# Performance work log

Hardware: AMD Instinct MI355X
Metric: run time of the kernel (lower is better)

## Reference

```python
import jax, jax.numpy as jnp
import numpy as np


def setup_inputs() -> dict:
    key = jax.random.key(0)
    ks = jax.random.split(key, 7)
    T, K, D_x, D_y = 8192, 64, 128, 64
    X = jax.random.normal(ks[0], (T, D_x), dtype=jnp.float32)
    Y = jax.random.normal(ks[1], (T, D_y), dtype=jnp.float32)
    # learned parameters (small random values for non-degenerate math)
    init_logits = jax.random.normal(ks[2], (K,), dtype=jnp.float32) * 0.1
    W = jax.random.normal(ks[3], (K, K, D_x), dtype=jnp.float32) * 0.05
    b = jax.random.normal(ks[4], (K, K), dtype=jnp.float32) * 0.1
    mu = jax.random.normal(ks[5], (K, D_y), dtype=jnp.float32) * 0.1
    log_var_unconstrained = jax.random.normal(ks[6], (K, D_y), dtype=jnp.float32) * 0.1
    return {"X": X, "Y": Y, "init_logits": init_logits, "W": W, "b": b,
            "mu": mu, "log_var_unconstrained": log_var_unconstrained}


def reference(X, Y, init_logits, W, b, mu, log_var_unconstrained):
    # log pi0
    log_pi0 = jax.nn.log_softmax(init_logits)
    # emissions for all t: diagonal Gaussian log-pdf, log_em [T, K]
    log_var = jnp.clip(log_var_unconstrained, -6.0, 6.0)  # [K, D_y]
    D = Y.shape[-1]
    LOG2PI = jnp.log(jnp.asarray(2.0 * np.pi, dtype=Y.dtype))
    diff = Y[:, None, :] - mu[None, :, :]                 # [T, K, D_y]
    quad = jnp.sum(diff * diff * jnp.exp(-log_var)[None], axis=-1)  # [T, K]
    logdet = jnp.sum(log_var, axis=-1)                    # [K]
    log_em = -0.5 * (D * LOG2PI + logdet[None, :] + quad)  # [T, K]
    # time-varying transition logits: b_ij + x_t . W_ij, row-softmax over j
    logits = b[None, :, :] + jnp.einsum('ijd,td->tij', W, X)  # [T, K, K]
    log_A = jax.nn.log_softmax(logits, axis=2)                 # [T, K, K]
    # forward recursion: alpha_t(j) = log_em_t(j) + logsumexp_i(alpha_{t-1}(i) + log_A_t(i,j))
    alpha0 = log_pi0 + log_em[0]

    def step(alpha, inputs):
        log_A_t, log_em_t = inputs
        alpha_new = log_em_t + jax.nn.logsumexp(alpha[:, None] + log_A_t, axis=0)
        return alpha_new, None

    alpha_T, _ = jax.lax.scan(step, alpha0, (log_A[1:], log_em[1:]))
    loglik = jax.nn.logsumexp(alpha_T)
    return loglik
```

## Files before the change

### kernel.cpp

```cpp
#include <hip/hip_runtime.h>
#include <hip/hip_bf16.h>


typedef unsigned int u32;
typedef unsigned short u16;

#define T_LEN 8192

typedef __attribute__((ext_vector_type(8))) short bf16x8;
typedef __attribute__((ext_vector_type(4))) float f32x4;

__device__ __forceinline__ float bflo(u32 u){ return __uint_as_float(u << 16); }
__device__ __forceinline__ float bfhi(u32 u){ return __uint_as_float(u & 0xffff0000u); }
__device__ __forceinline__ u32 f2bf(float x){
  u32 b = __float_as_uint(x);
  return (b + 0x7fffu + ((b >> 16) & 1u)) >> 16;
}
__device__ __forceinline__ u32 pack2bf(float a, float b){
  return f2bf(a) | (f2bf(b) << 16);
}

#if defined(__has_builtin)
#if __has_builtin(__builtin_amdgcn_fdot2_f32_bf16)
#define HAVE_DOT2 1
#endif
#endif

#if HAVE_DOT2
typedef __attribute__((ext_vector_type(2))) __bf16 bf16v2;
__device__ __forceinline__ float dot2bf(u32 a, u32 b, float c){
  return __builtin_amdgcn_fdot2_f32_bf16(
      __builtin_bit_cast(bf16v2, a), __builtin_bit_cast(bf16v2, b), c, false);
}
#else
__device__ __forceinline__ float dot2bf(u32 a, u32 b, float c){
  return fmaf(bfhi(a), bfhi(b), fmaf(bflo(a), bflo(b), c));
}
#endif

__global__ __launch_bounds__(64) void k_prep(
    const float* __restrict__ mu, const float* __restrict__ lvu,
    float* __restrict__ muT, float* __restrict__ ivT, float* __restrict__ logdet)
{
  const int k = threadIdx.x;
  float ld = 0.f;
  for (int d = 0; d < 64; ++d){
    float lv = fminf(fmaxf(lvu[k*64 + d], -6.f), 6.f);
    ld += lv;
    muT[d*64 + k] = mu[k*64 + d];
    ivT[d*64 + k] = __expf(-lv);
  }
  logdet[k] = ld;
}

__global__ __launch_bounds__(256) void k_emis(
    const float* __restrict__ Y, const float* __restrict__ muT,
    const float* __restrict__ ivT, const float* __restrict__ logdet,
    float* __restrict__ emp, float* __restrict__ cvec)
{
  const int w = threadIdx.x >> 6, k = threadIdx.x & 63;
  const int t = blockIdx.x * 4 + w;
  float y = Y[(size_t)t*64 + k];
  float quad = 0.f;
  #pragma unroll 8
  for (int d = 0; d < 64; ++d){
    float yd = __shfl(y, d, 64);
    float df = yd - muT[d*64 + k];
    quad = fmaf(df*df, ivT[d*64 + k], quad);
  }
  float le = -0.5f*(117.6241322f + logdet[k] + quad);
  float m = le;
  #pragma unroll
  for (int off = 1; off < 64; off <<= 1) m = fmaxf(m, __shfl_xor(m, off, 64));
  emp[(size_t)t*64 + k] = __expf(le - m);
  if (k == 0) cvec[t] = m;
}

__global__ __launch_bounds__(256) void k_trans(
    const float* __restrict__ X, const float* __restrict__ W,
    const float* __restrict__ bmat, const float* __restrict__ emp,
    u16* __restrict__ Ap)
{
  __shared__ __align__(16) u16 Xs[128*128];
  __shared__ __align__(16) u16 Ws[64*128];
  const int tid = threadIdx.x;
  const int t0 = blockIdx.x * 128;
  const int i  = blockIdx.y;

  {
    const float4* xs = (const float4*)(X + (size_t)t0 * 128);
    #pragma unroll
    for (int u = 0; u < 16; ++u){
      int f = u*256 + tid;
      float4 v = xs[f];
      int row = f >> 5, c = f & 31;
      int byte = (row*256 + c*8) ^ ((row & 7) << 4);
      *(uint2*)((char*)Xs + byte) = make_uint2(pack2bf(v.x, v.y), pack2bf(v.z, v.w));
    }
    const float4* wsrc = (const float4*)(W + (size_t)i * 8192);
    #pragma unroll
    for (int u = 0; u < 8; ++u){
      int f = u*256 + tid;
      float4 v = wsrc[f];
      int row = f >> 5, c = f & 31;
      int byte = (row*256 + c*8) ^ ((row & 7) << 4);
      *(uint2*)((char*)Ws + byte) = make_uint2(pack2bf(v.x, v.y), pack2bf(v.z, v.w));
    }
  }
  __syncthreads();

  const int lane = tid & 63, w = tid >> 6;
  const int lr = lane & 15, lg = lane >> 4;

  f32x4 acc[2][4] = {};
  #pragma unroll
  for (int kg = 0; kg < 4; ++kg){
    const int kbyte = kg*64 + lg*16;
    bf16x8 a[2], b[4];
    #pragma unroll
    for (int mt = 0; mt < 2; ++mt){
      int row = w*32 + mt*16 + lr;
      a[mt] = *(const bf16x8*)((const char*)Xs + ((row*256 + kbyte) ^ ((row&7)<<4)));
    }
    #pragma unroll
    for (int nt = 0; nt < 4; ++nt){
      int row = nt*16 + lr;
      b[nt] = *(const bf16x8*)((const char*)Ws + ((row*256 + kbyte) ^ ((row&7)<<4)));
    }
    #pragma unroll
    for (int mt = 0; mt < 2; ++mt)
      #pragma unroll
      for (int nt = 0; nt < 4; ++nt)
        acc[mt][nt] = __builtin_amdgcn_mfma_f32_16x16x32_bf16(a[mt], b[nt], acc[mt][nt], 0, 0, 0);
  }

  float bv[4];
  #pragma unroll
  for (int nt = 0; nt < 4; ++nt) bv[nt] = bmat[i*64 + nt*16 + lr];

  #pragma unroll
  for (int mt = 0; mt < 2; ++mt){
    #pragma unroll
    for (int reg = 0; reg < 4; ++reg){
      const int t = t0 + w*32 + mt*16 + lg*4 + reg;
      float v0 = acc[mt][0][reg] + bv[0];
      float v1 = acc[mt][1][reg] + bv[1];
      float v2 = acc[mt][2][reg] + bv[2];
      float v3 = acc[mt][3][reg] + bv[3];
      float mx = fmaxf(fmaxf(v0,v1), fmaxf(v2,v3));
      #pragma unroll
      for (int off = 1; off < 16; off <<= 1) mx = fmaxf(mx, __shfl_xor(mx, off, 64));
      float e0 = __expf(v0-mx), e1 = __expf(v1-mx), e2 = __expf(v2-mx), e3 = __expf(v3-mx);
      float sum = e0 + e1 + e2 + e3;
      #pragma unroll
      for (int off = 1; off < 16; off <<= 1) sum += __shfl_xor(sum, off, 64);
      float inv = 1.0f / sum;
      const float* er = emp + (size_t)t*64;
      u16* op = Ap + (size_t)t*4096 + i*64;
      op[ 0 + lr] = (u16)f2bf(e0*inv*er[ 0 + lr]);
      op[16 + lr] = (u16)f2bf(e1*inv*er[16 + lr]);
      op[32 + lr] = (u16)f2bf(e2*inv*er[32 + lr]);
      op[48 + lr] = (u16)f2bf(e3*inv*er[48 + lr]);
    }
  }
}

__global__ __launch_bounds__(256) void k_scan(
    u16* mats, int mstride, int per_wg, int skip0,
    const float* __restrict__ in_sc, float* __restrict__ out_sc)
{
  __shared__ u32 Apk[2][32][64];
  const int tid = threadIdx.x;
  const int lane = tid & 63, w = tid >> 6;
  const int r = lane & 15, g = lane >> 4;
  int c0 = blockIdx.x * per_wg, cnt = per_wg;
  const size_t out_slot = (size_t)c0 * mstride;
  if (blockIdx.x == 0){ c0 += skip0; cnt -= skip0; }

  u32 M[8];
  {
    const uint4* mp0 = (const uint4*)(mats + ((size_t)c0*mstride << 12) + ((w*16 + r) << 6) + (g << 4));
    uint4 a = mp0[0], b = mp0[1];
    M[0]=a.x; M[1]=a.y; M[2]=a.z; M[3]=a.w;
    M[4]=b.x; M[5]=b.y; M[6]=b.z; M[7]=b.w;
  }
  float S = in_sc ? in_sc[c0*4 + w] : 0.0f;

  const int lp = tid >> 3, c8 = tid & 7;
  auto STAGE = [&](int buf, const u16* src){
    const uint4 A = *(const uint4*)(src + lp*128 + c8*8);
    const uint4 B = *(const uint4*)(src + lp*128 + 64 + c8*8);
    uint4 o0, o1;
    o0.x = (A.x & 0xffffu) | (B.x << 16);
    o0.y = (A.x >> 16)     | (B.x & 0xffff0000u);
    o0.z = (A.y & 0xffffu) | (B.y << 16);
    o0.w = (A.y >> 16)     | (B.y & 0xffff0000u);
    o1.x = (A.z & 0xffffu) | (B.z << 16);
    o1.y = (A.z >> 16)     | (B.z & 0xffff0000u);
    o1.z = (A.w & 0xffffu) | (B.w << 16);
    o1.w = (A.w >> 16)     | (B.w & 0xffff0000u);
    const int s = lp & 7;
    *(uint4*)&Apk[buf][lp][((2*c8    ) ^ s) << 2] = o0;
    *(uint4*)&Apk[buf][lp][((2*c8 + 1) ^ s) << 2] = o1;
  };

  if (cnt > 1) STAGE(0, mats + ((size_t)(c0+1)*mstride << 12));
  __syncthreads();
  int cur = 0;
  for (int kk = 1; kk < cnt; ++kk){
    if (kk + 1 < cnt) STAGE(cur ^ 1, mats + ((size_t)(c0 + kk + 1)*mstride << 12));

    if (in_sc){
      const float* sp = in_sc + (size_t)(c0 + kk)*4;
      float s0=sp[0], s1=sp[1], s2=sp[2], s3=sp[3];
      float sm = fmaxf(fmaxf(s0,s1), fmaxf(s2,s3));
      float se = __expf(sp[g] - sm);
      S += sm;
      #pragma unroll
      for (int q = 0; q < 8; ++q)
        M[q] = pack2bf(bflo(M[q])*se, bfhi(M[q])*se);
    }

    float acc[16];
    #pragma unroll
    for (int c = 0; c < 16; ++c) acc[c] = 0.f;
    const u32* Ab = &Apk[cur][0][0];
    #pragma unroll
    for (int p = 0; p < 32; ++p){
      u32 mp = __shfl(M[p & 7], r + ((p >> 3) << 4), 64);
      const u32* Ar = Ab + p*64;
      #pragma unroll
      for (int k4 = 0; k4 < 4; ++k4){
        uint4 av = *(const uint4*)(Ar + ((((g<<2) + k4) ^ (p & 7)) << 2));
        acc[k4*4+0] = dot2bf(mp, av.x, acc[k4*4+0]);
        acc[k4*4+1] = dot2bf(mp, av.y, acc[k4*4+1]);
        acc[k4*4+2] = dot2bf(mp, av.z, acc[k4*4+2]);
        acc[k4*4+3] = dot2bf(mp, av.w, acc[k4*4+3]);
      }
    }
    float mx = acc[0];
    #pragma unroll
    for (int c = 1; c < 16; ++c) mx = fmaxf(mx, acc[c]);
    #pragma unroll
    for (int off = 1; off < 64; off <<= 1) mx = fmaxf(mx, __shfl_xor(mx, off, 64));
    float inv = 1.0f / mx;
    S += __logf(mx);
    #pragma unroll
    for (int q = 0; q < 8; ++q)
      M[q] = pack2bf(acc[2*q]*inv, acc[2*q+1]*inv);
    cur ^= 1;
    __syncthreads();
  }
  {
    uint4* outp = (uint4*)(mats + (out_slot << 12) + ((w*16 + r) << 6) + (g << 4));
    uint4 a, b;
    a.x=M[0]; a.y=M[1]; a.z=M[2]; a.w=M[3];
    b.x=M[4]; b.y=M[5]; b.z=M[6]; b.w=M[7];
    outp[0] = a; outp[1] = b;
    if (lane == 0) out_sc[blockIdx.x*4 + w] = S;
  }
}

__global__ __launch_bounds__(256) void k_final(
    const float* __restrict__ init_logits, const float* __restrict__ emp,
    const float* __restrict__ cvec, const u16* __restrict__ Mfin, int mstride,
    const float* __restrict__ scfin, int nmat, float* __restrict__ out)
{
  __shared__ float wsum[4];
  const int tid = threadIdx.x;
  float part = 0.f;
  for (int t = tid; t < T_LEN; t += 256) part += cvec[t];
  #pragma unroll
  for (int off = 1; off < 64; off <<= 1) part += __shfl_xor(part, off, 64);
  if ((tid & 63) == 0) wsum[tid >> 6] = part;
  __syncthreads();
  if (tid >= 64) return;
  const float csum = wsum[0] + wsum[1] + wsum[2] + wsum[3];
  const int k = tid;
  float ilv = init_logits[k];
  float m = ilv;
  #pragma unroll
  for (int off = 1; off < 64; off <<= 1) m = fmaxf(m, __shfl_xor(m, off, 64));
  float e = __expf(ilv - m);
  float s = e;
  #pragma unroll
  for (int off = 1; off < 64; off <<= 1) s += __shfl_xor(s, off, 64);
  float alpha = (e / s) * emp[k];
  float S = 0.f;
  for (int d = 0; d < nmat; ++d){
    const float* sp = scfin + d*4;
    float sm = fmaxf(fmaxf(sp[0], sp[1]), fmaxf(sp[2], sp[3]));
    alpha *= __expf(sp[k >> 4] - sm);
    S += sm;
    const u16* Mp = Mfin + ((size_t)d*mstride << 12);
    float an = 0.f;
    for (int i2 = 0; i2 < 64; ++i2){
      float av = __shfl(alpha, i2, 64);
      an = fmaf(av, __uint_as_float(((u32)Mp[i2*64 + k]) << 16), an);
    }
    float mx = an;
    #pragma unroll
    for (int off = 1; off < 64; off <<= 1) mx = fmaxf(mx, __shfl_xor(mx, off, 64));
    alpha = an / mx;
    S += __logf(mx);
  }
  float tot = alpha;
  #pragma unroll
  for (int off = 1; off < 64; off <<= 1) tot += __shfl_xor(tot, off, 64);
  if (k == 0) out[0] = __logf(tot) + S + csum;
}

extern "C" void kernel_launch(void* const* d_in, const int* in_sizes, int n_in,
                              void* d_out, int out_size, void* d_ws, size_t ws_size,
                              hipStream_t stream)
{
  const float* X  = (const float*)d_in[0];
  const float* Y  = (const float*)d_in[1];
  const float* il = (const float*)d_in[2];
  const float* W  = (const float*)d_in[3];
  const float* bm = (const float*)d_in[4];
  const float* mu = (const float*)d_in[5];
  const float* lv = (const float*)d_in[6];
  float* out = (float*)d_out;
  char* ws = (char*)d_ws;
  (void)in_sizes; (void)n_in; (void)out_size; (void)ws_size;

  float* emp    = (float*)(ws + 0x0000000);
  float* cvec   = (float*)(ws + 0x0200000);
  float* muT    = (float*)(ws + 0x0210000);
  float* ivT    = (float*)(ws + 0x0214000);
  float* logdet = (float*)(ws + 0x0218000);
  float* sc1    = (float*)(ws + 0x0220000);
  float* sc2    = (float*)(ws + 0x0224000);
  float* sc3    = (float*)(ws + 0x0225000);
  float* sc4    = (float*)(ws + 0x0226000);
  float* sc5    = (float*)(ws + 0x0227000);
  u16*   Ap     = (u16*)  (ws + 0x0400000);

  k_prep <<<1, 64, 0, stream>>>(mu, lv, muT, ivT, logdet);
  k_emis <<<2048, 256, 0, stream>>>(Y, muT, ivT, logdet, emp, cvec);
  k_trans<<<dim3(64, 64), 256, 0, stream>>>(X, W, bm, emp, Ap);
  k_scan <<<1024, 256, 0, stream>>>(Ap,   1, 8, 1, (const float*)nullptr, sc1);
  k_scan <<<256,  256, 0, stream>>>(Ap,   8, 4, 0, sc1, sc2);
  k_scan <<<64,   256, 0, stream>>>(Ap,  32, 4, 0, sc2, sc3);
  k_scan <<<16,   256, 0, stream>>>(Ap, 128, 4, 0, sc3, sc4);
  k_scan <<<4,    256, 0, stream>>>(Ap, 512, 4, 0, sc4, sc5);
  k_final<<<1, 256, 0, stream>>>(il, emp, cvec, Ap, 2048, sc5, 4, out);
}
```

Measured before the change: 237.1 us.

## Use MFMA for scan matrix products and stage transition writes through LDS

After: 196.2 us. 1.21x faster.

```diff
diff --git a/kernel.cpp b/kernel.cpp
--- a/kernel.cpp
+++ b/kernel.cpp
@@ -19,24 +19,6 @@
 __device__ __forceinline__ u32 pack2bf(float a, float b){
   return f2bf(a) | (f2bf(b) << 16);
 }
-
-#if defined(__has_builtin)
-#if __has_builtin(__builtin_amdgcn_fdot2_f32_bf16)
-#define HAVE_DOT2 1
-#endif
-#endif
-
-#if HAVE_DOT2
-typedef __attribute__((ext_vector_type(2))) __bf16 bf16v2;
-__device__ __forceinline__ float dot2bf(u32 a, u32 b, float c){
-  return __builtin_amdgcn_fdot2_f32_bf16(
-      __builtin_bit_cast(bf16v2, a), __builtin_bit_cast(bf16v2, b), c, false);
-}
-#else
-__device__ __forceinline__ float dot2bf(u32 a, u32 b, float c){
-  return fmaf(bfhi(a), bfhi(b), fmaf(bflo(a), bflo(b), c));
-}
-#endif
 
 __global__ __launch_bounds__(64) void k_prep(
     const float* __restrict__ mu, const float* __restrict__ lvu,
@@ -138,11 +120,15 @@
   #pragma unroll
   for (int nt = 0; nt < 4; ++nt) bv[nt] = bmat[i*64 + nt*16 + lr];
 
+  __syncthreads();
+  u16* Ct = Xs;
+
   #pragma unroll
   for (int mt = 0; mt < 2; ++mt){
     #pragma unroll
     for (int reg = 0; reg < 4; ++reg){
-      const int t = t0 + w*32 + mt*16 + lg*4 + reg;
+      const int row = w*32 + mt*16 + lg*4 + reg;
+      const int t = t0 + row;
       float v0 = acc[mt][0][reg] + bv[0];
       float v1 = acc[mt][1][reg] + bv[1];
       float v2 = acc[mt][2][reg] + bv[2];
@@ -156,12 +142,20 @@
       for (int off = 1; off < 16; off <<= 1) sum += __shfl_xor(sum, off, 64);
       float inv = 1.0f / sum;
       const float* er = emp + (size_t)t*64;
-      u16* op = Ap + (size_t)t*4096 + i*64;
-      op[ 0 + lr] = (u16)f2bf(e0*inv*er[ 0 + lr]);
-      op[16 + lr] = (u16)f2bf(e1*inv*er[16 + lr]);
-      op[32 + lr] = (u16)f2bf(e2*inv*er[32 + lr]);
-      op[48 + lr] = (u16)f2bf(e3*inv*er[48 + lr]);
-    }
+      const int sw = (row & 7) << 4;
+      *(u16*)((char*)Ct + row*128 + ((( 0 + lr)*2) ^ sw)) = (u16)f2bf(e0*inv*er[ 0 + lr]);
+      *(u16*)((char*)Ct + row*128 + (((16 + lr)*2) ^ sw)) = (u16)f2bf(e1*inv*er[16 + lr]);
+      *(u16*)((char*)Ct + row*128 + (((32 + lr)*2) ^ sw)) = (u16)f2bf(e2*inv*er[32 + lr]);
+      *(u16*)((char*)Ct + row*128 + (((48 + lr)*2) ^ sw)) = (u16)f2bf(e3*inv*er[48 + lr]);
+    }
+  }
+  __syncthreads();
+  #pragma unroll
+  for (int q = 0; q < 4; ++q){
+    const int f = tid*4 + q;
+    const int row = f >> 3, c = f & 7;
+    uint4 v = *(const uint4*)((const char*)Ct + row*128 + ((c*16) ^ ((row & 7) << 4)));
+    *(uint4*)(Ap + (size_t)(t0 + row)*4096 + (size_t)i*64 + c*8) = v;
   }
 }
 
@@ -169,20 +163,19 @@
     u16* mats, int mstride, int per_wg, int skip0,
     const float* __restrict__ in_sc, float* __restrict__ out_sc)
 {
-  __shared__ u32 Apk[2][32][64];
+  __shared__ u32 Apk[2][32*68];
   const int tid = threadIdx.x;
   const int lane = tid & 63, w = tid >> 6;
-  const int r = lane & 15, g = lane >> 4;
+  const int r16 = lane & 15, oct = lane >> 4;
   int c0 = blockIdx.x * per_wg, cnt = per_wg;
   const size_t out_slot = (size_t)c0 * mstride;
   if (blockIdx.x == 0){ c0 += skip0; cnt -= skip0; }
 
-  u32 M[8];
+  bf16x8 Bf[2];
   {
-    const uint4* mp0 = (const uint4*)(mats + ((size_t)c0*mstride << 12) + ((w*16 + r) << 6) + (g << 4));
-    uint4 a = mp0[0], b = mp0[1];
-    M[0]=a.x; M[1]=a.y; M[2]=a.z; M[3]=a.w;
-    M[4]=b.x; M[5]=b.y; M[6]=b.z; M[7]=b.w;
+    const u16* m0 = mats + ((size_t)c0*mstride << 12) + (w*16 + r16)*64 + oct*8;
+    Bf[0] = *(const bf16x8*)(m0);
+    Bf[1] = *(const bf16x8*)(m0 + 32);
   }
   float S = in_sc ? in_sc[c0*4 + w] : 0.0f;
 
@@ -199,9 +192,9 @@
     o1.y = (A.z >> 16)     | (B.z & 0xffff0000u);
     o1.z = (A.w & 0xffffu) | (B.w << 16);
     o1.w = (A.w >> 16)     | (B.w & 0xffff0000u);
-    const int s = lp & 7;
-    *(uint4*)&Apk[buf][lp][((2*c8    ) ^ s) << 2] = o0;
-    *(uint4*)&Apk[buf][lp][((2*c8 + 1) ^ s) << 2] = o1;
+    u32* dst = &Apk[buf][lp*68 + c8*8];
+    *(uint4*)(dst)     = o0;
+    *(uint4*)(dst + 4) = o1;
   };
 
   if (cnt > 1) STAGE(0, mats + ((size_t)(c0+1)*mstride << 12));
@@ -214,49 +207,73 @@
       const float* sp = in_sc + (size_t)(c0 + kk)*4;
       float s0=sp[0], s1=sp[1], s2=sp[2], s3=sp[3];
       float sm = fmaxf(fmaxf(s0,s1), fmaxf(s2,s3));
-      float se = __expf(sp[g] - sm);
       S += sm;
       #pragma unroll
-      for (int q = 0; q < 8; ++q)
-        M[q] = pack2bf(bflo(M[q])*se, bfhi(M[q])*se);
-    }
-
-    float acc[16];
-    #pragma unroll
-    for (int c = 0; c < 16; ++c) acc[c] = 0.f;
-    const u32* Ab = &Apk[cur][0][0];
-    #pragma unroll
-    for (int p = 0; p < 32; ++p){
-      u32 mp = __shfl(M[p & 7], r + ((p >> 3) << 4), 64);
-      const u32* Ar = Ab + p*64;
-      #pragma unroll
-      for (int k4 = 0; k4 < 4; ++k4){
-        uint4 av = *(const uint4*)(Ar + ((((g<<2) + k4) ^ (p & 7)) << 2));
-        acc[k4*4+0] = dot2bf(mp, av.x, acc[k4*4+0]);
-        acc[k4*4+1] = dot2bf(mp, av.y, acc[k4*4+1]);
-        acc[k4*4+2] = dot2bf(mp, av.z, acc[k4*4+2]);
-        acc[k4*4+3] = dot2bf(mp, av.w, acc[k4*4+3]);
+      for (int kt = 0; kt < 2; ++kt){
+        float slo = (kt == 0) ? s0 : s2;
+        float shi = (kt == 0) ? s1 : s3;
+        float se = __expf(((oct >> 1) ? shi : slo) - sm);
+        uint4 bv4 = __builtin_bit_cast(uint4, Bf[kt]);
+        bv4.x = pack2bf(bflo(bv4.x)*se, bfhi(bv4.x)*se);
+        bv4.y = pack2bf(bflo(bv4.y)*se, bfhi(bv4.y)*se);
+        bv4.z = pack2bf(bflo(bv4.z)*se, bfhi(bv4.z)*se);
+        bv4.w = pack2bf(bflo(bv4.w)*se, bfhi(bv4.w)*se);
+        Bf[kt] = __builtin_bit_cast(bf16x8, bv4);
       }
     }
-    float mx = acc[0];
-    #pragma unroll
-    for (int c = 1; c < 16; ++c) mx = fmaxf(mx, acc[c]);
+
+    f32x4 acc[4] = {};
+    const u32* Ab = &Apk[cur][0];
+    #pragma unroll
+    for (int kt = 0; kt < 2; ++kt){
+      const u32* gb = Ab + (kt*16 + oct*4)*68 + r16;
+      #pragma unroll
+      for (int jt = 0; jt < 4; ++jt){
+        const u32* g = gb + jt*16;
+        uint4 av = make_uint4(g[0], g[68], g[136], g[204]);
+        acc[jt] = __builtin_amdgcn_mfma_f32_16x16x32_bf16(
+            __builtin_bit_cast(bf16x8, av), Bf[kt], acc[jt], 0, 0, 0);
+      }
+    }
+
+    float mx = acc[0][0];
+    #pragma unroll
+    for (int jt = 0; jt < 4; ++jt)
+      #pragma unroll
+      for (int q = 0; q < 4; ++q) mx = fmaxf(mx, acc[jt][q]);
     #pragma unroll
     for (int off = 1; off < 64; off <<= 1) mx = fmaxf(mx, __shfl_xor(mx, off, 64));
     float inv = 1.0f / mx;
     S += __logf(mx);
-    #pragma unroll
-    for (int q = 0; q < 8; ++q)
-      M[q] = pack2bf(acc[2*q]*inv, acc[2*q+1]*inv);
+
+    u32 p0[4], p1[4];
+    #pragma unroll
+    for (int jt = 0; jt < 4; ++jt){
+      p0[jt] = pack2bf(acc[jt][0]*inv, acc[jt][1]*inv);
+      p1[jt] = pack2bf(acc[jt][2]*inv, acc[jt][3]*inv);
+    }
+    const int s0l = r16 + 32*(oct & 1), s1l = s0l + 16;
+    const bool hi = (oct >> 1) != 0;
+    #pragma unroll
+    for (int kt = 0; kt < 2; ++kt){
+      u32 a0 = __shfl(p0[2*kt],   s0l, 64), a1 = __shfl(p1[2*kt],   s0l, 64);
+      u32 a2 = __shfl(p0[2*kt],   s1l, 64), a3 = __shfl(p1[2*kt],   s1l, 64);
+      u32 b0 = __shfl(p0[2*kt+1], s0l, 64), b1 = __shfl(p1[2*kt+1], s0l, 64);
+      u32 b2 = __shfl(p0[2*kt+1], s1l, 64), b3 = __shfl(p1[2*kt+1], s1l, 64);
+      uint4 nb;
+      nb.x = hi ? b0 : a0;
+      nb.y = hi ? b1 : a1;
+      nb.z = hi ? b2 : a2;
+      nb.w = hi ? b3 : a3;
+      Bf[kt] = __builtin_bit_cast(bf16x8, nb);
+    }
     cur ^= 1;
     __syncthreads();
   }
   {
-    uint4* outp = (uint4*)(mats + (out_slot << 12) + ((w*16 + r) << 6) + (g << 4));
-    uint4 a, b;
-    a.x=M[0]; a.y=M[1]; a.z=M[2]; a.w=M[3];
-    b.x=M[4]; b.y=M[5]; b.z=M[6]; b.w=M[7];
-    outp[0] = a; outp[1] = b;
+    u16* outp = mats + (out_slot << 12) + (w*16 + r16)*64 + oct*8;
+    *(bf16x8*)(outp)      = Bf[0];
+    *(bf16x8*)(outp + 32) = Bf[1];
     if (lane == 0) out_sc[blockIdx.x*4 + w] = S;
   }
 }
```
